# Optimization experiments

Measured on AMD Instinct MI355X. Metric: run time of the kernel, lower is better.

The kernel has to match this reference:

```python
import jax, jax.numpy as jnp
import numpy as np

# Grid / physics constants (stand-ins for the attributes of self.model)
N = 256                 # voxels per axis (cubic unit cell)
CELL = 100.0            # unit cell edge in Angstrom (orthogonal cell, frac matrix = I/CELL)
SPACING = CELL / N      # voxel spacing in Angstrom
SOLVENT_R = 1.1         # dilation probe radius (init default `radius`)
EROSION_R = 0.9         # erosion radius (init default `erosion_radius`)
VDW_MAX = 1.9           # static upper bound on vdw radii (generation range [1.2,1.9])
N_ATOMS = 5000


def setup_inputs() -> dict:
    key = jax.random.key(0)
    k1, k2 = jax.random.split(key)
    xyz = jax.random.uniform(k1, (N_ATOMS, 3), jnp.float32) * CELL
    vdw_radii = 1.2 + 0.7 * jax.random.uniform(k2, (N_ATOMS,), jnp.float32)
    return {"xyz": xyz, "vdw_radii": vdw_radii}


def _solvent_pipeline(xyz, vdw_radii):
    # ---- Step 1: dilation -- per-atom radius query into the voxel grid ----
    max_r = VDW_MAX + SOLVENT_R                       # self.max_radius_angstrom
    Kh = int(np.ceil(max_r / SPACING))
    g = np.arange(-Kh, Kh + 1)
    offs = np.stack(np.meshgrid(g, g, g, indexing='ij'), -1).reshape(-1, 3)
    offs = jnp.asarray(offs, jnp.int32)               # [M,3] local voxel offsets

    base = jnp.floor(xyz / SPACING).astype(jnp.int32)          # [A,3] home voxel
    coords = base[:, None, :] + offs[None, :, :]               # [A,M,3]
    centers = coords.astype(jnp.float32) * SPACING             # voxel centers (unwrapped)
    d = jnp.sqrt(jnp.sum((centers - xyz[:, None, :]) ** 2, -1))  # [A,M] atom-voxel dist

    w = jnp.mod(coords, N)                                     # periodic wrap of indices
    flat = ((w[..., 0] * N + w[..., 1]) * N + w[..., 2]).ravel()

    vr = vdw_radii[:, None]
    prot = (d < vr).ravel()                                    # inside vdw -> protein core
    bound = ((d >= vr) & (d < vr + SOLVENT_R)).ravel()         # vdw..vdw+probe -> boundary

    protein = (jnp.zeros(N ** 3, jnp.int8).at[flat].max(prot.astype(jnp.int8)) > 0)
    boundary = (jnp.zeros(N ** 3, jnp.int8).at[flat].max(bound.astype(jnp.int8)) > 0)
    protein = protein.reshape(N, N, N)
    boundary = boundary.reshape(N, N, N) & ~protein            # symmetry = identity (P1)
    def_solv = ~(protein | boundary)

    # ---- Step 2: erosion -- boundary voxel flips to solvent if any voxel within
    #      erosion_radius is definitely solvent ----
    rh = int(np.ceil(EROSION_R / SPACING))
    g2 = np.arange(-rh, rh + 1)
    eo = np.stack(np.meshgrid(g2, g2, g2, indexing='ij'), -1).reshape(-1, 3)
    eo = eo[np.linalg.norm(eo * SPACING, axis=1) <= EROSION_R]  # sphere stencil (static)
    has_nb = jnp.zeros((N, N, N), bool)
    for o in eo:  # small static stencil (~50 offsets)
        has_nb = has_nb | jnp.roll(def_solv, shift=(-int(o[0]), -int(o[1]), -int(o[2])), axis=(0, 1, 2))
    flip = boundary & has_nb
    protein_with_boundary = (protein | boundary) & ~flip
    solvent = (~protein_with_boundary).astype(jnp.float32)

    # ---- Step 3: Gaussian smoothing with circular padding ----
    sigma = (SOLVENT_R / SPACING) / 4.0                        # self.transition (voxels)
    ks = int(4 * sigma + 1)
    if ks % 2 == 0:
        ks += 1
    x = np.arange(ks) - ks // 2
    g1 = np.exp(-x ** 2 / (2 * sigma ** 2))
    g1 = g1 / g1.sum()
    k3 = g1[:, None, None] * g1[None, :, None] * g1[None, None, :]
    k3 = jnp.asarray(k3 / k3.sum(), jnp.float32)
    pad = ks // 2
    padded = jnp.pad(solvent, pad, mode='wrap')
    out = jax.lax.conv_general_dilated(padded[None, None], k3[None, None], (1, 1, 1), 'VALID')
    return out[0, 0]  # [N,N,N] smoothed solvent mask


def reference(xyz, vdw_radii):
    return _solvent_pipeline(xyz, vdw_radii)
```

## Files before the change

### kernel.cpp

```cpp
#include <hip/hip_runtime.h>
#include <math.h>

#define NG 256
#define NG3 (NG*NG*NG)
#define NW (NG3/64)

typedef unsigned long long u64;
typedef unsigned int u32;

constexpr float SPACING_F = 0.390625f;
constexpr int KH = 8;
constexpr int KD = 17;
constexpr int NPAIR = KD * KD;

#define CB(x, y) (((((x) & 255) << 8) | ((y) & 255)) << 2)

__global__ void __launch_bounds__(256) splat_bits_kernel(
    const float* __restrict__ xyz, const float* __restrict__ vdw,
    u64* __restrict__ occ_bits, u64* __restrict__ p_bits, int natoms)
{
    int t = blockIdx.x * 256 + threadIdx.x;
    if (t >= natoms * NPAIR) return;
    int atom = t / NPAIR;
    int pr = t - atom * NPAIR;
    int dx = pr / KD - KH;
    int dy = pr - (pr / KD) * KD - KH;

    const float ax = xyz[atom * 3 + 0];
    const float ay = xyz[atom * 3 + 1];
    const float az = xyz[atom * 3 + 2];
    const float vr = vdw[atom];
    const float br = __fadd_rn(vr, 1.1f);
    const int bx = (int)floorf(__fdiv_rn(ax, SPACING_F));
    const int by = (int)floorf(__fdiv_rn(ay, SPACING_F));
    const int bz = (int)floorf(__fdiv_rn(az, SPACING_F));

    const int cx = bx + dx, cy = by + dy;
    float ex = __fsub_rn(__fmul_rn((float)cx, SPACING_F), ax);
    float ey = __fsub_rn(__fmul_rn((float)cy, SPACING_F), ay);
    float rxy2 = __fadd_rn(__fmul_rn(ex, ex), __fmul_rn(ey, ey));
    if (rxy2 >= __fmul_rn(br, br)) return;

    u32 mo = 0, mp = 0;
    #pragma unroll
    for (int k = 0; k < KD; ++k) {
        int cz = bz + k - KH;
        float ez = __fsub_rn(__fmul_rn((float)cz, SPACING_F), az);
        float s = __fadd_rn(rxy2, __fmul_rn(ez, ez));
        float d = __fsqrt_rn(s);
        mo |= (d < br) ? (1u << k) : 0u;
        mp |= (d < vr) ? (1u << k) : 0u;
    }
    if (!mo) return;

    const int cb = CB(cx, cy);
    const int zA = (bz - KH) & 255;
    const int wa = zA >> 6;
    const int off = zA & 63;

    u64 lo = (u64)mo << off;
    u64 hi = off ? ((u64)mo >> (64 - off)) : 0ULL;
    if (lo) atomicOr(&occ_bits[cb | wa], lo);
    if (hi) atomicOr(&occ_bits[cb | ((wa + 1) & 3)], hi);
    if (mp) {
        u64 plo = (u64)mp << off;
        u64 phi = off ? ((u64)mp >> (64 - off)) : 0ULL;
        if (plo) atomicOr(&p_bits[cb | wa], plo);
        if (phi) atomicOr(&p_bits[cb | ((wa + 1) & 3)], phi);
    }
}

__device__ __forceinline__ u64 rng5(const u64* __restrict__ B, int cb, int wz) {
    u64 C = B[cb | wz], P = B[cb | ((wz + 3) & 3)], Nw = B[cb | ((wz + 1) & 3)];
    u64 d1 = (C << 1) | (P >> 63), d2 = (C << 2) | (P >> 62);
    u64 u1 = (C >> 1) | (Nw << 63), u2 = (C >> 2) | (Nw << 62);
    return C & d1 & d2 & u1 & u2;
}
__device__ __forceinline__ u64 rng3(const u64* __restrict__ B, int cb, int wz) {
    u64 C = B[cb | wz], P = B[cb | ((wz + 3) & 3)], Nw = B[cb | ((wz + 1) & 3)];
    u64 d1 = (C << 1) | (P >> 63);
    u64 u1 = (C >> 1) | (Nw << 63);
    return C & d1 & u1;
}

__global__ void __launch_bounds__(256) solvent_bits_kernel(
    const u64* __restrict__ occ_bits, const u64* __restrict__ p_bits,
    u64* __restrict__ sol_bits)
{
    int w = blockIdx.x * 256 + threadIdx.x;
    int wz = w & 3, col = w >> 2;
    int y = col & 255, x = col >> 8;

    u64 ero = rng5(occ_bits, CB(x, y), wz);
    ero &= rng5(occ_bits, CB(x + 1, y), wz);
    ero &= rng5(occ_bits, CB(x - 1, y), wz);
    ero &= rng5(occ_bits, CB(x, y + 1), wz);
    ero &= rng5(occ_bits, CB(x, y - 1), wz);
    ero &= rng3(occ_bits, CB(x + 1, y + 1), wz);
    ero &= rng3(occ_bits, CB(x + 1, y - 1), wz);
    ero &= rng3(occ_bits, CB(x - 1, y + 1), wz);
    ero &= rng3(occ_bits, CB(x - 1, y - 1), wz);
    ero &= rng3(occ_bits, CB(x + 2, y), wz);
    ero &= rng3(occ_bits, CB(x - 2, y), wz);
    ero &= rng3(occ_bits, CB(x, y + 2), wz);
    ero &= rng3(occ_bits, CB(x, y - 2), wz);
    ero &= occ_bits[CB(x + 1, y + 2) | wz];
    ero &= occ_bits[CB(x + 1, y - 2) | wz];
    ero &= occ_bits[CB(x - 1, y + 2) | wz];
    ero &= occ_bits[CB(x - 1, y - 2) | wz];
    ero &= occ_bits[CB(x + 2, y + 1) | wz];
    ero &= occ_bits[CB(x + 2, y - 1) | wz];
    ero &= occ_bits[CB(x - 2, y + 1) | wz];
    ero &= occ_bits[CB(x - 2, y - 1) | wz];

    u64 occw = occ_bits[w];
    u64 pw = p_bits[w];
    sol_bits[w] = ~(pw | (occw & ero));
}

struct Tri { u64 m1, m0, p1; };
__device__ __forceinline__ Tri tri(const u64* __restrict__ B, int x, int y, int wz) {
    int cb = CB(x, y);
    u64 C = B[cb | wz], P = B[cb | ((wz + 3) & 3)], Nw = B[cb | ((wz + 1) & 3)];
    Tri t;
    t.m0 = C;
    t.m1 = (C << 1) | (P >> 63);
    t.p1 = (C >> 1) | (Nw << 63);
    return t;
}

__device__ __forceinline__ void csa(u64 a, u64 b, u64 c, u64& s, u64& cy) {
    u64 t = a ^ b;
    s = t ^ c;
    cy = (a & b) | (t & c);
}

__global__ void __launch_bounds__(256) gauss_bits_kernel(
    const u64* __restrict__ S, float* __restrict__ out,
    float W0, float W1, float W2, float W3)
{
    __shared__ float lutA[256];
    __shared__ float lds[256][33];
    const int tid = threadIdx.x;
    {
        int g = tid & 1, c1v = (tid >> 1) & 7, c2v = (tid >> 4) & 15;
        float acc = g ? W0 : 0.0f;
        acc = fmaf(W1, (float)c1v, acc);
        acc = fmaf(W2, (float)c2v, acc);
        lutA[tid] = acc;
    }
    __syncthreads();

    const int w = blockIdx.x * 256 + tid;
    const int wz = w & 3, col = w >> 2;
    const int y = col & 255, x = col >> 8;

    Tri cc = tri(S, x, y, wz);
    Tri e0 = tri(S, x + 1, y, wz), e1 = tri(S, x - 1, y, wz);
    Tri e2 = tri(S, x, y + 1, wz), e3 = tri(S, x, y - 1, wz);
    Tri d0 = tri(S, x + 1, y + 1, wz), d1 = tri(S, x + 1, y - 1, wz);
    Tri d2 = tri(S, x - 1, y + 1, wz), d3 = tri(S, x - 1, y - 1, wz);

    u64 sa, ca, sb, cb2;
    csa(cc.m1, cc.p1, e0.m0, sa, ca);
    csa(e1.m0, e2.m0, e3.m0, sb, cb2);
    u64 c1b0 = sa ^ sb; u64 h = sa & sb;
    u64 c1b1, c1b2;
    csa(ca, cb2, h, c1b1, c1b2);

    u64 s1, k1, s2, k2, s3, k3, s4, k4;
    csa(e0.m1, e0.p1, e1.m1, s1, k1);
    csa(e1.p1, e2.m1, e2.p1, s2, k2);
    csa(e3.m1, e3.p1, d0.m0, s3, k3);
    csa(d1.m0, d2.m0, d3.m0, s4, k4);
    u64 t5, kt;
    csa(s1, s2, s3, t5, kt);
    u64 c2b0 = t5 ^ s4; u64 h0 = t5 & s4;
    u64 u_, ku, v_, kv;
    csa(k1, k2, k3, u_, ku);
    csa(k4, kt, h0, v_, kv);
    u64 c2b1 = u_ ^ v_; u64 h1 = u_ & v_;
    u64 c2b2, c2b3;
    csa(ku, kv, h1, c2b2, c2b3);

    u64 p1s, p1c, p2s, p2c;
    csa(d0.m1, d0.p1, d1.m1, p1s, p1c);
    csa(d1.p1, d2.m1, d2.p1, p2s, p2c);
    u64 t3, kt3;
    csa(p1s, p2s, d3.m1, t3, kt3);
    u64 c3b0 = t3 ^ d3.p1; u64 h3 = t3 & d3.p1;
    u64 u3, ku3;
    csa(p1c, p2c, kt3, u3, ku3);
    u64 c3b1 = u3 ^ h3; u64 h4 = u3 & h3;
    u64 c3b2 = ku3 ^ h4, c3b3 = ku3 & h4;

    float* blk_out = out + (size_t)blockIdx.x * 256 * 64;

    #pragma unroll
    for (int hh = 0; hh < 2; ++hh) {
        const int sh = hh * 32;
        u32 pA[8] = { (u32)(cc.m0 >> sh), (u32)(c1b0 >> sh), (u32)(c1b1 >> sh),
                      (u32)(c1b2 >> sh), (u32)(c2b0 >> sh), (u32)(c2b1 >> sh),
                      (u32)(c2b2 >> sh), (u32)(c2b3 >> sh) };
        u32 pB[4] = { (u32)(c3b0 >> sh), (u32)(c3b1 >> sh),
                      (u32)(c3b2 >> sh), (u32)(c3b3 >> sh) };
        #pragma unroll
        for (int z0 = 0; z0 < 8; ++z0) {
            u32 accA = 0, accB = 0;
            #pragma unroll
            for (int j = 0; j < 8; ++j) accA |= ((pA[j] >> z0) & 0x01010101u) << j;
            #pragma unroll
            for (int j = 0; j < 4; ++j) accB |= ((pB[j] >> z0) & 0x01010101u) << j;
            #pragma unroll
            for (int b = 0; b < 4; ++b) {
                int idxA = (accA >> (8 * b)) & 255;
                int c3v  = (accB >> (8 * b)) & 15;
                float val = fmaf(W3, (float)c3v, lutA[idxA]);
                lds[tid][z0 + 8 * b] = val;
            }
        }
        __syncthreads();
        #pragma unroll
        for (int k = 0; k < 8; ++k) {
            int i = tid + k * 256;
            int wl = i >> 3;
            int zo = (i & 7) * 4;
            float4 v = make_float4(lds[wl][zo], lds[wl][zo + 1],
                                   lds[wl][zo + 2], lds[wl][zo + 3]);
            *(float4*)(blk_out + (size_t)wl * 64 + sh + zo) = v;
        }
        __syncthreads();
    }
}

extern "C" void kernel_launch(void* const* d_in, const int* in_sizes, int n_in,
                              void* d_out, int out_size, void* d_ws, size_t ws_size,
                              hipStream_t stream)
{
    const float* xyz = (const float*)d_in[0];
    const float* vdw = (const float*)d_in[1];
    float* out = (float*)d_out;

    u64* occ_bits = (u64*)d_ws;
    u64* p_bits   = occ_bits + NW;
    u64* sol_bits = p_bits + NW;
    const int natoms = in_sizes[1];

    hipMemsetAsync(occ_bits, 0, 2 * NW * sizeof(u64), stream);

    int nthreads = natoms * NPAIR;
    splat_bits_kernel<<<(nthreads + 255) / 256, 256, 0, stream>>>(
        xyz, vdw, occ_bits, p_bits, natoms);
    solvent_bits_kernel<<<NW / 256, 256, 0, stream>>>(occ_bits, p_bits, sol_bits);

    double spacing = 100.0 / 256.0;
    double sigma = 1.1 / spacing / 4.0;
    double a = exp(-1.0 / (2.0 * sigma * sigma));
    double ssum = 2.0 * a + 1.0;
    double an = a / ssum, bn = 1.0 / ssum;
    float W0 = (float)(bn * bn * bn);
    float W1 = (float)(an * bn * bn);
    float W2 = (float)(an * an * bn);
    float W3 = (float)(an * an * an);

    gauss_bits_kernel<<<NW / 256, 256, 0, stream>>>(sol_bits, out, W0, W1, W2, W3);
}
```

Baseline: 119.8 us.

## Replace atom scatter splat with binned per-tile gather into LDS bitmasks

Atoms are first binned into a 64x64 xy grid, then each block owns a 16x16 column tile, gathers candidate atoms from nearby bins, queues passing (atom, column) pairs, and ORs z-bitmasks into shared memory before writing the tile out with vector stores. This removes the large global memset and the many global 64-bit atomics of the scatter approach. Fixed caps (32 atoms per bin, 160 candidates, 8192 queue entries) can silently drop atoms in dense regions, which risks wrong output for clustered inputs. Only 256 blocks are launched, so parallelism is lower.

Result: slower. 134.9 us (+12.6%).

```diff
diff --git a/kernel.cpp b/kernel.cpp
--- a/kernel.cpp
+++ b/kernel.cpp
@@ -7,66 +7,159 @@
 
 typedef unsigned long long u64;
 typedef unsigned int u32;
+typedef unsigned short u16;
 
 constexpr float SPACING_F = 0.390625f;
 constexpr int KH = 8;
 constexpr int KD = 17;
-constexpr int NPAIR = KD * KD;
+
+#define NBIN 64
+#define BCAP 32
+#define NCAND 160
+#define QCAP 8192
 
 #define CB(x, y) (((((x) & 255) << 8) | ((y) & 255)) << 2)
 
-__global__ void __launch_bounds__(256) splat_bits_kernel(
+__global__ void bin_fill_kernel(const float* __restrict__ xyz, int natoms,
+                                int* __restrict__ bin_cnt, int* __restrict__ bin_list)
+{
+    int a = blockIdx.x * 256 + threadIdx.x;
+    if (a >= natoms) return;
+    float ax = xyz[a * 3 + 0], ay = xyz[a * 3 + 1];
+    int bx = (int)floorf(__fdiv_rn(ax, SPACING_F));
+    int by = (int)floorf(__fdiv_rn(ay, SPACING_F));
+    int b = ((by >> 2) & (NBIN - 1)) * NBIN + ((bx >> 2) & (NBIN - 1));
+    int s = atomicAdd(&bin_cnt[b], 1);
+    if (s < BCAP) bin_list[b * BCAP + s] = a;
+}
+
+__global__ void __launch_bounds__(256) gather_splat_kernel(
     const float* __restrict__ xyz, const float* __restrict__ vdw,
-    u64* __restrict__ occ_bits, u64* __restrict__ p_bits, int natoms)
-{
-    int t = blockIdx.x * 256 + threadIdx.x;
-    if (t >= natoms * NPAIR) return;
-    int atom = t / NPAIR;
-    int pr = t - atom * NPAIR;
-    int dx = pr / KD - KH;
-    int dy = pr - (pr / KD) * KD - KH;
-
-    const float ax = xyz[atom * 3 + 0];
-    const float ay = xyz[atom * 3 + 1];
-    const float az = xyz[atom * 3 + 2];
-    const float vr = vdw[atom];
-    const float br = __fadd_rn(vr, 1.1f);
-    const int bx = (int)floorf(__fdiv_rn(ax, SPACING_F));
-    const int by = (int)floorf(__fdiv_rn(ay, SPACING_F));
-    const int bz = (int)floorf(__fdiv_rn(az, SPACING_F));
-
-    const int cx = bx + dx, cy = by + dy;
-    float ex = __fsub_rn(__fmul_rn((float)cx, SPACING_F), ax);
-    float ey = __fsub_rn(__fmul_rn((float)cy, SPACING_F), ay);
-    float rxy2 = __fadd_rn(__fmul_rn(ex, ex), __fmul_rn(ey, ey));
-    if (rxy2 >= __fmul_rn(br, br)) return;
-
-    u32 mo = 0, mp = 0;
+    const int* __restrict__ bin_cnt, const int* __restrict__ bin_list,
+    u64* __restrict__ occ_bits, u64* __restrict__ p_bits)
+{
+    __shared__ float4 candF[NCAND];
+    __shared__ int4   candI[NCAND];
+    __shared__ u32 occT[2048];
+    __shared__ u32 pT[2048];
+    __shared__ u16 queue[QCAP];
+    __shared__ int lc, qn;
+
+    const int tid = threadIdx.x;
+    const int BX = blockIdx.x & 15, BY = blockIdx.x >> 4;
+    const int x0 = BX * 16, y0 = BY * 16;
+    const int lx = tid & 15, ly = tid >> 4;
+    const int X = x0 + lx, Y = y0 + ly;
+    const int lane = tid & 63;
+
+    if (tid == 0) { lc = 0; qn = 0; }
     #pragma unroll
-    for (int k = 0; k < KD; ++k) {
-        int cz = bz + k - KH;
-        float ez = __fsub_rn(__fmul_rn((float)cz, SPACING_F), az);
-        float s = __fadd_rn(rxy2, __fmul_rn(ez, ez));
-        float d = __fsqrt_rn(s);
-        mo |= (d < br) ? (1u << k) : 0u;
-        mp |= (d < vr) ? (1u << k) : 0u;
-    }
-    if (!mo) return;
-
-    const int cb = CB(cx, cy);
-    const int zA = (bz - KH) & 255;
-    const int wa = zA >> 6;
-    const int off = zA & 63;
-
-    u64 lo = (u64)mo << off;
-    u64 hi = off ? ((u64)mo >> (64 - off)) : 0ULL;
-    if (lo) atomicOr(&occ_bits[cb | wa], lo);
-    if (hi) atomicOr(&occ_bits[cb | ((wa + 1) & 3)], hi);
-    if (mp) {
-        u64 plo = (u64)mp << off;
-        u64 phi = off ? ((u64)mp >> (64 - off)) : 0ULL;
-        if (plo) atomicOr(&p_bits[cb | wa], plo);
-        if (phi) atomicOr(&p_bits[cb | ((wa + 1) & 3)], phi);
+    for (int k = 0; k < 8; ++k) { occT[tid + k * 256] = 0; pT[tid + k * 256] = 0; }
+    __syncthreads();
+
+    if (tid < 64) {
+        int abx = (4 * BX - 2 + (tid & 7)) & (NBIN - 1);
+        int aby = (4 * BY - 2 + (tid >> 3)) & (NBIN - 1);
+        int b = aby * NBIN + abx;
+        int n = min(bin_cnt[b], BCAP);
+        if (n > 0) {
+            int base = atomicAdd(&lc, n);
+            for (int j = 0; j < n; ++j) {
+                int idx = base + j;
+                if (idx < NCAND) {
+                    int a = bin_list[b * BCAP + j];
+                    float ax = xyz[a * 3 + 0], ay = xyz[a * 3 + 1], az = xyz[a * 3 + 2];
+                    candF[idx] = make_float4(ax, ay, az, vdw[a]);
+                    int bx = (int)floorf(__fdiv_rn(ax, SPACING_F));
+                    int by = (int)floorf(__fdiv_rn(ay, SPACING_F));
+                    int bz = (int)floorf(__fdiv_rn(az, SPACING_F));
+                    candI[idx] = make_int4(bx, by, bz, 0);
+                }
+            }
+        }
+    }
+    __syncthreads();
+    const int nc = min(lc, NCAND);
+
+    for (int c = 0; c < nc; ++c) {
+        float4 f = candF[c];
+        int4 bi = candI[c];
+        int dx = ((X - bi.x + 128) & 255) - 128;
+        int dy = ((Y - bi.y + 128) & 255) - 128;
+        bool pass = false;
+        if (dx >= -KH && dx <= KH && dy >= -KH && dy <= KH) {
+            float ex = __fsub_rn(__fmul_rn((float)(bi.x + dx), SPACING_F), f.x);
+            float ey = __fsub_rn(__fmul_rn((float)(bi.y + dy), SPACING_F), f.y);
+            float rxy2 = __fadd_rn(__fmul_rn(ex, ex), __fmul_rn(ey, ey));
+            float br = __fadd_rn(f.w, 1.1f);
+            pass = rxy2 < __fmul_rn(br, br);
+        }
+        u64 bal = __ballot(pass);
+        if (bal) {
+            int leader = __ffsll((long long)bal) - 1;
+            int base = 0;
+            if (lane == leader) base = atomicAdd(&qn, __popcll(bal));
+            base = __shfl(base, leader, 64);
+            if (pass) {
+                int r = __popcll(bal & ((1ull << lane) - 1ull));
+                int q = base + r;
+                if (q < QCAP) queue[q] = (u16)((c << 8) | tid);
+            }
+        }
+    }
+    __syncthreads();
+    const int nq = min(qn, QCAP);
+
+    for (int q = tid; q < nq; q += 256) {
+        u16 e = queue[q];
+        int c = e >> 8, col = e & 255;
+        float4 f = candF[c];
+        int4 bi = candI[c];
+        int clx = col & 15, cly = col >> 4;
+        int dx = (((x0 + clx) - bi.x + 128) & 255) - 128;
+        int dy = (((y0 + cly) - bi.y + 128) & 255) - 128;
+        float ex = __fsub_rn(__fmul_rn((float)(bi.x + dx), SPACING_F), f.x);
+        float ey = __fsub_rn(__fmul_rn((float)(bi.y + dy), SPACING_F), f.y);
+        float rxy2 = __fadd_rn(__fmul_rn(ex, ex), __fmul_rn(ey, ey));
+        float vr = f.w;
+        float br = __fadd_rn(vr, 1.1f);
+        u32 mo = 0, mp = 0;
+        #pragma unroll
+        for (int k = 0; k < KD; ++k) {
+            int cz = bi.z + k - KH;
+            float ez = __fsub_rn(__fmul_rn((float)cz, SPACING_F), f.z);
+            float s = __fadd_rn(rxy2, __fmul_rn(ez, ez));
+            float d = __fsqrt_rn(s);
+            mo |= (d < br) ? (1u << k) : 0u;
+            mp |= (d < vr) ? (1u << k) : 0u;
+        }
+        if (!mo) continue;
+        int zA = (bi.z - KH) & 255;
+        int base32 = clx * 128 + cly * 8;
+        int w0 = zA >> 5, off = zA & 31;
+        u64 m = (u64)mo << off;
+        u32 lo = (u32)m, hi = (u32)(m >> 32);
+        if (lo) atomicOr(&occT[base32 + w0], lo);
+        if (hi) atomicOr(&occT[base32 + ((w0 + 1) & 7)], hi);
+        if (mp) {
+            u64 pm = (u64)mp << off;
+            u32 plo = (u32)pm, phi = (u32)(pm >> 32);
+            if (plo) atomicOr(&pT[base32 + w0], plo);
+            if (phi) atomicOr(&pT[base32 + ((w0 + 1) & 7)], phi);
+        }
+    }
+    __syncthreads();
+
+    u32* og = (u32*)occ_bits;
+    u32* pg = (u32*)p_bits;
+    #pragma unroll
+    for (int k = 0; k < 2; ++k) {
+        int i = tid * 4 + k * 1024;
+        int xx = i >> 7;
+        int rem = i & 127;
+        u32 gbase = ((u32)(x0 + xx) << 11) + ((u32)y0 << 3) + (u32)rem;
+        *(uint4*)(og + gbase) = make_uint4(occT[i], occT[i+1], occT[i+2], occT[i+3]);
+        *(uint4*)(pg + gbase) = make_uint4(pT[i], pT[i+1], pT[i+2], pT[i+3]);
     }
 }
 
@@ -244,13 +337,15 @@
     u64* occ_bits = (u64*)d_ws;
     u64* p_bits   = occ_bits + NW;
     u64* sol_bits = p_bits + NW;
+    int* bin_cnt  = (int*)(sol_bits + NW);
+    int* bin_list = bin_cnt + NBIN * NBIN;
     const int natoms = in_sizes[1];
 
-    hipMemsetAsync(occ_bits, 0, 2 * NW * sizeof(u64), stream);
-
-    int nthreads = natoms * NPAIR;
-    splat_bits_kernel<<<(nthreads + 255) / 256, 256, 0, stream>>>(
-        xyz, vdw, occ_bits, p_bits, natoms);
+    hipMemsetAsync(bin_cnt, 0, NBIN * NBIN * sizeof(int), stream);
+    bin_fill_kernel<<<(natoms + 255) / 256, 256, 0, stream>>>(
+        xyz, natoms, bin_cnt, bin_list);
+    gather_splat_kernel<<<256, 256, 0, stream>>>(
+        xyz, vdw, bin_cnt, bin_list, occ_bits, p_bits);
     solvent_bits_kernel<<<NW / 256, 256, 0, stream>>>(occ_bits, p_bits, sol_bits);
 
     double spacing = 100.0 / 256.0;
```

## Fuse erosion and Gaussian passes into one tiled kernel with shared-memory halos

Applied to the files above, without the earlier changes.

Merges the solvent-bit erosion kernel and the Gaussian bit-count kernel into a single kernel. Each block handles an 8x8 xy tile: it loads a 14x14 occupancy halo into shared memory, computes a 10x10 solvent-bit tile there, then runs the 3x3x3 Gaussian from shared memory. This removes one kernel launch and the global write and re-read of the solvent bit array. In exchange it recomputes erosion on halo columns, and the output stores become strided per tile instead of fully contiguous per block.

Measured after the change: 113.6 us (median of 2 runs). 1.06x faster.

```diff
diff --git a/kernel.cpp b/kernel.cpp
--- a/kernel.cpp
+++ b/kernel.cpp
@@ -70,58 +70,30 @@
     }
 }
 
-__device__ __forceinline__ u64 rng5(const u64* __restrict__ B, int cb, int wz) {
-    u64 C = B[cb | wz], P = B[cb | ((wz + 3) & 3)], Nw = B[cb | ((wz + 1) & 3)];
+#define LCB(ox, oy) ((((ox) * 14) + (oy)) * 4)
+#define SCB(sx, sy) ((((sx) * 10) + (sy)) * 4)
+
+union SMem {
+    u64 occT[784];
+    float stage[256][33];
+};
+
+__device__ __forceinline__ u64 lrng5(const u64* T, int cb, int wz) {
+    u64 C = T[cb | wz], P = T[cb | ((wz + 3) & 3)], Nw = T[cb | ((wz + 1) & 3)];
     u64 d1 = (C << 1) | (P >> 63), d2 = (C << 2) | (P >> 62);
     u64 u1 = (C >> 1) | (Nw << 63), u2 = (C >> 2) | (Nw << 62);
     return C & d1 & d2 & u1 & u2;
 }
-__device__ __forceinline__ u64 rng3(const u64* __restrict__ B, int cb, int wz) {
-    u64 C = B[cb | wz], P = B[cb | ((wz + 3) & 3)], Nw = B[cb | ((wz + 1) & 3)];
+__device__ __forceinline__ u64 lrng3(const u64* T, int cb, int wz) {
+    u64 C = T[cb | wz], P = T[cb | ((wz + 3) & 3)], Nw = T[cb | ((wz + 1) & 3)];
     u64 d1 = (C << 1) | (P >> 63);
     u64 u1 = (C >> 1) | (Nw << 63);
     return C & d1 & u1;
 }
 
-__global__ void __launch_bounds__(256) solvent_bits_kernel(
-    const u64* __restrict__ occ_bits, const u64* __restrict__ p_bits,
-    u64* __restrict__ sol_bits)
-{
-    int w = blockIdx.x * 256 + threadIdx.x;
-    int wz = w & 3, col = w >> 2;
-    int y = col & 255, x = col >> 8;
-
-    u64 ero = rng5(occ_bits, CB(x, y), wz);
-    ero &= rng5(occ_bits, CB(x + 1, y), wz);
-    ero &= rng5(occ_bits, CB(x - 1, y), wz);
-    ero &= rng5(occ_bits, CB(x, y + 1), wz);
-    ero &= rng5(occ_bits, CB(x, y - 1), wz);
-    ero &= rng3(occ_bits, CB(x + 1, y + 1), wz);
-    ero &= rng3(occ_bits, CB(x + 1, y - 1), wz);
-    ero &= rng3(occ_bits, CB(x - 1, y + 1), wz);
-    ero &= rng3(occ_bits, CB(x - 1, y - 1), wz);
-    ero &= rng3(occ_bits, CB(x + 2, y), wz);
-    ero &= rng3(occ_bits, CB(x - 2, y), wz);
-    ero &= rng3(occ_bits, CB(x, y + 2), wz);
-    ero &= rng3(occ_bits, CB(x, y - 2), wz);
-    ero &= occ_bits[CB(x + 1, y + 2) | wz];
-    ero &= occ_bits[CB(x + 1, y - 2) | wz];
-    ero &= occ_bits[CB(x - 1, y + 2) | wz];
-    ero &= occ_bits[CB(x - 1, y - 2) | wz];
-    ero &= occ_bits[CB(x + 2, y + 1) | wz];
-    ero &= occ_bits[CB(x + 2, y - 1) | wz];
-    ero &= occ_bits[CB(x - 2, y + 1) | wz];
-    ero &= occ_bits[CB(x - 2, y - 1) | wz];
-
-    u64 occw = occ_bits[w];
-    u64 pw = p_bits[w];
-    sol_bits[w] = ~(pw | (occw & ero));
-}
-
 struct Tri { u64 m1, m0, p1; };
-__device__ __forceinline__ Tri tri(const u64* __restrict__ B, int x, int y, int wz) {
-    int cb = CB(x, y);
-    u64 C = B[cb | wz], P = B[cb | ((wz + 3) & 3)], Nw = B[cb | ((wz + 1) & 3)];
+__device__ __forceinline__ Tri triL(const u64* T, int cb, int wz) {
+    u64 C = T[cb | wz], P = T[cb | ((wz + 3) & 3)], Nw = T[cb | ((wz + 1) & 3)];
     Tri t;
     t.m0 = C;
     t.m1 = (C << 1) | (P >> 63);
@@ -135,13 +107,23 @@
     cy = (a & b) | (t & c);
 }
 
-__global__ void __launch_bounds__(256) gauss_bits_kernel(
-    const u64* __restrict__ S, float* __restrict__ out,
-    float W0, float W1, float W2, float W3)
+__global__ void __launch_bounds__(256) solv_gauss_kernel(
+    const u64* __restrict__ occ_bits, const u64* __restrict__ p_bits,
+    float* __restrict__ out, float W0, float W1, float W2, float W3)
 {
+    __shared__ SMem sm;
+    __shared__ u64 solT[400];
     __shared__ float lutA[256];
-    __shared__ float lds[256][33];
+
     const int tid = threadIdx.x;
+    const int bx = blockIdx.x & 31, by = blockIdx.x >> 5;
+    const int x0 = bx * 8, y0 = by * 8;
+
+    for (int i = tid; i < 784; i += 256) {
+        int owz = i & 3; int c = i >> 2;
+        int oy = c % 14, ox = c / 14;
+        sm.occT[i] = occ_bits[CB(x0 - 3 + ox, y0 - 3 + oy) | owz];
+    }
     {
         int g = tid & 1, c1v = (tid >> 1) & 7, c2v = (tid >> 4) & 15;
         float acc = g ? W0 : 0.0f;
@@ -151,15 +133,49 @@
     }
     __syncthreads();
 
-    const int w = blockIdx.x * 256 + tid;
-    const int wz = w & 3, col = w >> 2;
-    const int y = col & 255, x = col >> 8;
-
-    Tri cc = tri(S, x, y, wz);
-    Tri e0 = tri(S, x + 1, y, wz), e1 = tri(S, x - 1, y, wz);
-    Tri e2 = tri(S, x, y + 1, wz), e3 = tri(S, x, y - 1, wz);
-    Tri d0 = tri(S, x + 1, y + 1, wz), d1 = tri(S, x + 1, y - 1, wz);
-    Tri d2 = tri(S, x - 1, y + 1, wz), d3 = tri(S, x - 1, y - 1, wz);
+    for (int i = tid; i < 400; i += 256) {
+        int swz = i & 3; int c = i >> 2;
+        int sy = c % 10, sx = c / 10;
+        int ox = sx + 2, oy = sy + 2;
+        const u64* T = sm.occT;
+        u64 ero = lrng5(T, LCB(ox, oy), swz);
+        ero &= lrng5(T, LCB(ox + 1, oy), swz);
+        ero &= lrng5(T, LCB(ox - 1, oy), swz);
+        ero &= lrng5(T, LCB(ox, oy + 1), swz);
+        ero &= lrng5(T, LCB(ox, oy - 1), swz);
+        ero &= lrng3(T, LCB(ox + 1, oy + 1), swz);
+        ero &= lrng3(T, LCB(ox + 1, oy - 1), swz);
+        ero &= lrng3(T, LCB(ox - 1, oy + 1), swz);
+        ero &= lrng3(T, LCB(ox - 1, oy - 1), swz);
+        ero &= lrng3(T, LCB(ox + 2, oy), swz);
+        ero &= lrng3(T, LCB(ox - 2, oy), swz);
+        ero &= lrng3(T, LCB(ox, oy + 2), swz);
+        ero &= lrng3(T, LCB(ox, oy - 2), swz);
+        ero &= T[LCB(ox + 1, oy + 2) | swz];
+        ero &= T[LCB(ox + 1, oy - 2) | swz];
+        ero &= T[LCB(ox - 1, oy + 2) | swz];
+        ero &= T[LCB(ox - 1, oy - 2) | swz];
+        ero &= T[LCB(ox + 2, oy + 1) | swz];
+        ero &= T[LCB(ox + 2, oy - 1) | swz];
+        ero &= T[LCB(ox - 2, oy + 1) | swz];
+        ero &= T[LCB(ox - 2, oy - 1) | swz];
+
+        u64 C = T[LCB(ox, oy) | swz];
+        u64 pw = p_bits[CB(x0 - 1 + sx, y0 - 1 + sy) | swz];
+        solT[i] = ~(pw | (C & ero));
+    }
+    __syncthreads();
+
+    const int gwz = tid & 3;
+    const int gc = tid >> 2;
+    const int gy = gc & 7, gx = gc >> 3;
+    const int sx = gx + 1, sy = gy + 1;
+
+    Tri cc = triL(solT, SCB(sx, sy), gwz);
+    Tri e0 = triL(solT, SCB(sx + 1, sy), gwz), e1 = triL(solT, SCB(sx - 1, sy), gwz);
+    Tri e2 = triL(solT, SCB(sx, sy + 1), gwz), e3 = triL(solT, SCB(sx, sy - 1), gwz);
+    Tri d0 = triL(solT, SCB(sx + 1, sy + 1), gwz), d1 = triL(solT, SCB(sx + 1, sy - 1), gwz);
+    Tri d2 = triL(solT, SCB(sx - 1, sy + 1), gwz), d3 = triL(solT, SCB(sx - 1, sy - 1), gwz);
 
     u64 sa, ca, sb, cb2;
     csa(cc.m1, cc.p1, e0.m0, sa, ca);
@@ -193,8 +209,6 @@
     csa(p1c, p2c, kt3, u3, ku3);
     u64 c3b1 = u3 ^ h3; u64 h4 = u3 & h3;
     u64 c3b2 = ku3 ^ h4, c3b3 = ku3 & h4;
-
-    float* blk_out = out + (size_t)blockIdx.x * 256 * 64;
 
     #pragma unroll
     for (int hh = 0; hh < 2; ++hh) {
@@ -216,7 +230,7 @@
                 int idxA = (accA >> (8 * b)) & 255;
                 int c3v  = (accB >> (8 * b)) & 15;
                 float val = fmaf(W3, (float)c3v, lutA[idxA]);
-                lds[tid][z0 + 8 * b] = val;
+                sm.stage[tid][z0 + 8 * b] = val;
             }
         }
         __syncthreads();
@@ -225,9 +239,11 @@
             int i = tid + k * 256;
             int wl = i >> 3;
             int zo = (i & 7) * 4;
-            float4 v = make_float4(lds[wl][zo], lds[wl][zo + 1],
-                                   lds[wl][zo + 2], lds[wl][zo + 3]);
-            *(float4*)(blk_out + (size_t)wl * 64 + sh + zo) = v;
+            int ggx = wl >> 5, ggy = (wl >> 2) & 7, ggwz = wl & 3;
+            size_t base = ((size_t)(((x0 + ggx) << 10) + (y0 + ggy) * 4 + ggwz)) * 64;
+            float4 v = make_float4(sm.stage[wl][zo], sm.stage[wl][zo + 1],
+                                   sm.stage[wl][zo + 2], sm.stage[wl][zo + 3]);
+            *(float4*)(out + base + sh + zo) = v;
         }
         __syncthreads();
     }
@@ -243,7 +259,6 @@
 
     u64* occ_bits = (u64*)d_ws;
     u64* p_bits   = occ_bits + NW;
-    u64* sol_bits = p_bits + NW;
     const int natoms = in_sizes[1];
 
     hipMemsetAsync(occ_bits, 0, 2 * NW * sizeof(u64), stream);
@@ -251,7 +266,6 @@
     int nthreads = natoms * NPAIR;
     splat_bits_kernel<<<(nthreads + 255) / 256, 256, 0, stream>>>(
         xyz, vdw, occ_bits, p_bits, natoms);
-    solvent_bits_kernel<<<NW / 256, 256, 0, stream>>>(occ_bits, p_bits, sol_bits);
 
     double spacing = 100.0 / 256.0;
     double sigma = 1.1 / spacing / 4.0;
@@ -263,5 +277,6 @@
     float W2 = (float)(an * an * bn);
     float W3 = (float)(an * an * an);
 
-    gauss_bits_kernel<<<NW / 256, 256, 0, stream>>>(sol_bits, out, W0, W1, W2, W3);
-}
+    solv_gauss_kernel<<<1024, 256, 0, stream>>>(
+        occ_bits, p_bits, out, W0, W1, W2, W3);
+}
```
